# Kernel tuning notes

Hardware: AMD Instinct MI355X
Metric: run time of the kernel (lower is better)

Reference implementation:

```python
import jax, jax.numpy as jnp
import numpy as np
from jax import lax

DN = ('NCHW', 'OIHW', 'NCHW')


def setup_inputs() -> dict:
    key = jax.random.key(0)
    k1, k2 = jax.random.split(key)
    inp = jax.random.normal(k1, (32, 512, 28, 28), dtype=jnp.float32)
    w = jax.random.normal(k2, (2000, 512, 1, 1), dtype=jnp.float32)
    return {"input": inp, "weights": w}


def reference(input, weights):
    # conv2d(input^2, ones_like(weights)): every output channel is identical
    # (all-ones kernel broadcast over out-channels), so compute the
    # patch/channel sum ONCE with a single-output-channel ones kernel and
    # broadcast — same math as the original, without P-fold redundancy.
    P, C, kh, kw = weights.shape
    ones1 = jnp.ones((1, C, kh, kw), dtype=input.dtype)
    input2_patch_sum = lax.conv_general_dilated(
        input * input, ones1, window_strides=(1, 1), padding='VALID',
        dimension_numbers=DN)  # [B, 1, H', W'], broadcasts over P

    weights2 = jnp.sum(weights * weights, axis=(1, 2, 3))  # [P]
    weights2 = weights2.reshape(-1, 1, 1)  # [P, 1, 1]

    input_weights = lax.conv_general_dilated(
        input, weights, window_strides=(1, 1), padding='VALID',
        dimension_numbers=DN)  # [B, P, H', W']

    output = input2_patch_sum - 2.0 * input_weights + weights2[None]
    return jax.nn.relu(output)
```

## Files before the change

kernel.cpp:

```cpp
#include <hip/hip_runtime.h>
#include <stdint.h>

constexpr int C_IN  = 512;
constexpr int HW    = 784;
constexpr int NB    = 32;
constexpr int M_TOT = NB * HW;
constexpr int N_TOT = 2000;
constexpr int NPAD  = 2048;
constexpr int IMG_STRIDE = C_IN * HW;
constexpr int OUT_BATCH  = N_TOT * HW;

constexpr int TBM = 256;
constexpr int TBN = 128;
constexpr int NKT = C_IN / 32;

constexpr int PREPA_BLOCKS = M_TOT / 64;
constexpr int PREPW_BLOCKS = NPAD / 4;

typedef __attribute__((ext_vector_type(8))) short bf16x8;
typedef __attribute__((ext_vector_type(4))) float f32x4;

__device__ __forceinline__ uint16_t f2bf(float f) {
    union { float f; uint32_t u; } x; x.f = f;
    return (uint16_t)((x.u + 0x8000u) >> 16);
}

__device__ __forceinline__ void gload_lds16(const void* g, void* l) {
    __builtin_amdgcn_global_load_lds(
        (const __attribute__((address_space(1))) void*)g,
        (__attribute__((address_space(3))) void*)l, 16, 0, 0);
}

__device__ __forceinline__ f32x4 nt_load4(const float* p) {
    return __builtin_nontemporal_load((const f32x4*)p);
}
__device__ __forceinline__ void nt_store4(float* p, f32x4 v) {
    __builtin_nontemporal_store(v, (f32x4*)p);
}

__global__ __launch_bounds__(256) void prep_kernel(const float* __restrict__ in,
                                                   const float* __restrict__ w,
                                                   short* __restrict__ Abf,
                                                   short* __restrict__ Wbf,
                                                   float* __restrict__ s2,
                                                   float* __restrict__ w2) {
    __shared__ __align__(16) char T[64 * 512 * 2];
    __shared__ float red[16][64];

    const int t = threadIdx.x;

    if (blockIdx.x >= PREPA_BLOCKS) {
        const int wv = t >> 6, lane = t & 63;
        const int p = (blockIdx.x - PREPA_BLOCKS) * 4 + wv;
        bf16x8 o = (bf16x8)0;
        float s = 0.f;
        if (p < N_TOT) {
            const float* base = w + (size_t)p * C_IN + lane * 8;
            f32x4 a = nt_load4(base);
            f32x4 c = nt_load4(base + 4);
            s = a[0]*a[0] + a[1]*a[1] + a[2]*a[2] + a[3]*a[3]
              + c[0]*c[0] + c[1]*c[1] + c[2]*c[2] + c[3]*c[3];
            o[0] = (short)f2bf(a[0]); o[1] = (short)f2bf(a[1]);
            o[2] = (short)f2bf(a[2]); o[3] = (short)f2bf(a[3]);
            o[4] = (short)f2bf(c[0]); o[5] = (short)f2bf(c[1]);
            o[6] = (short)f2bf(c[2]); o[7] = (short)f2bf(c[3]);
        }
        *(bf16x8*)(Wbf + (size_t)p * C_IN + lane * 8) = o;
#pragma unroll
        for (int off = 32; off; off >>= 1) s += __shfl_down(s, off);
        if (lane == 0) w2[p] = s;
        return;
    }

    const int q = t & 15;
    const int part = t >> 4;
    const int m0q = blockIdx.x * 64 + q * 4;
    const uint32_t b  = (uint32_t)m0q / 784u;
    const uint32_t hw = (uint32_t)m0q % 784u;
    const float* base = in + (size_t)b * IMG_STRIDE + hw;

    float acx = 0.f, acy = 0.f, acz = 0.f, acw = 0.f;
    const int c0 = part * 32;
#pragma unroll 4
    for (int c = c0; c < c0 + 32; ++c) {
        f32x4 v = nt_load4(base + (size_t)c * HW);
        acx = fmaf(v[0], v[0], acx);
        acy = fmaf(v[1], v[1], acy);
        acz = fmaf(v[2], v[2], acz);
        acw = fmaf(v[3], v[3], acw);
        uint16_t vals[4] = { f2bf(v[0]), f2bf(v[1]), f2bf(v[2]), f2bf(v[3]) };
        const uint32_t by0 = (uint32_t)(q * 4) * 1024u + (uint32_t)c * 2u;
#pragma unroll
        for (int j = 0; j < 4; ++j) {
            uint32_t bb = by0 + (uint32_t)j * 1024u;
            bb ^= ((bb >> 12) & 7u) << 4;
            *(uint16_t*)(T + bb) = vals[j];
        }
    }
    red[part][q * 4 + 0] = acx;
    red[part][q * 4 + 1] = acy;
    red[part][q * 4 + 2] = acz;
    red[part][q * 4 + 3] = acw;
    __syncthreads();
    if (t < 64) {
        float s = 0.f;
#pragma unroll
        for (int p = 0; p < 16; ++p) s += red[p][t];
        s2[blockIdx.x * 64 + t] = s;
    }
    short* dst = Abf + (size_t)blockIdx.x * 64 * 512;
#pragma unroll
    for (int i = 0; i < 16; ++i) {
        const int idx = i * 256 + t;
        const int row = idx >> 6, ch = idx & 63;
        uint32_t bb = (uint32_t)row * 1024u + (uint32_t)ch * 16u;
        bb ^= ((bb >> 12) & 7u) << 4;
        bf16x8 v = *(bf16x8*)(T + bb);
        *(bf16x8*)(dst + (size_t)row * 512 + ch * 8) = v;
    }
}

__global__ __launch_bounds__(256, 2) void gemm10_kernel(const short* __restrict__ Abf,
                                                        const short* __restrict__ Wbf,
                                                        const float* __restrict__ s2,
                                                        const float* __restrict__ w2,
                                                        float* __restrict__ out) {
    __shared__ __align__(16) char smem[3 * 24576];

    const int t = threadIdx.x;
    const int wv = t >> 6, lane = t & 63;
    const int lr = lane & 15, lg = lane >> 4;

    const int bid = blockIdx.x;
    const int bn = bid & 15;
    const int bm = bid >> 4;

    const short* Ap = Abf + (size_t)bm * TBM * C_IN;
    const short* Bp = Wbf + (size_t)bn * TBN * C_IN;

    const int srow = wv * 16 + (lane >> 2);
    const int sg   = (lane & 3) ^ ((lane >> 3) & 3);
    const short* AsrcL = Ap + (size_t)srow * C_IN + sg * 8;
    const short* BsrcL = Bp + (size_t)srow * C_IN + sg * 8;
    const int dst = t * 16;

    const int wm = (wv >> 1) * 128;
    const int wn = (wv & 1) * 64;

    const int slot  = lg ^ ((lr >> 1) & 3);
    const int abase = (wm + lr) * 64 + slot * 16;
    const int bbase = 16384 + (wn + lr) * 64 + slot * 16;

    f32x4 acc[8][4] = {};

#define STAGE(tt)                                                              \
    do {                                                                       \
        char* buf_ = smem + ((tt) % 3) * 24576;                                \
        const short* as_ = AsrcL + (tt) * 32;                                  \
        const short* bs_ = BsrcL + (tt) * 32;                                  \
        gload_lds16(as_,              buf_ + dst);                             \
        gload_lds16(as_ +  64 * C_IN, buf_ + 4096 + dst);                      \
        gload_lds16(as_ + 128 * C_IN, buf_ + 8192 + dst);                      \
        gload_lds16(as_ + 192 * C_IN, buf_ + 12288 + dst);                     \
        gload_lds16(bs_,              buf_ + 16384 + dst);                     \
        gload_lds16(bs_ +  64 * C_IN, buf_ + 20480 + dst);                     \
    } while (0)

    STAGE(0);
    STAGE(1);

#pragma unroll
    for (int kt = 0; kt < NKT; ++kt) {
        if (kt < NKT - 1) asm volatile("s_waitcnt vmcnt(6)" ::: "memory");
        else              asm volatile("s_waitcnt vmcnt(0)" ::: "memory");
        __builtin_amdgcn_sched_barrier(0);
        __builtin_amdgcn_s_barrier();
        __builtin_amdgcn_sched_barrier(0);

        if (kt + 2 < NKT) STAGE(kt + 2);

        const char* buf = smem + (kt % 3) * 24576;
        bf16x8 bfrag[4], afrag[8];
#pragma unroll
        for (int n = 0; n < 4; ++n)
            bfrag[n] = *(const bf16x8*)(buf + bbase + n * 1024);
#pragma unroll
        for (int m = 0; m < 8; ++m)
            afrag[m] = *(const bf16x8*)(buf + abase + m * 1024);

        __builtin_amdgcn_s_setprio(1);
#pragma unroll
        for (int m = 0; m < 8; ++m)
#pragma unroll
            for (int n = 0; n < 4; ++n)
                acc[m][n] = __builtin_amdgcn_mfma_f32_16x16x32_bf16(
                    afrag[m], bfrag[n], acc[m][n], 0, 0, 0);
        __builtin_amdgcn_s_setprio(0);
    }
#undef STAGE

    float wreg[4];
    int n_ok[4];
#pragma unroll
    for (int n = 0; n < 4; ++n) {
        const int n_o = bn * TBN + wn + n * 16 + lr;
        n_ok[n] = (n_o < N_TOT);
        wreg[n] = n_ok[n] ? w2[n_o] : 0.f;
    }
#pragma unroll
    for (int m = 0; m < 8; ++m) {
        const int m_r = bm * TBM + wm + m * 16 + lg * 4;
        const f32x4 s2v = *(const f32x4*)(s2 + m_r);
        const uint32_t ob  = (uint32_t)m_r / 784u;
        const uint32_t ohw = (uint32_t)m_r % 784u;
        float* obase = out + (size_t)ob * OUT_BATCH + ohw;
#pragma unroll
        for (int n = 0; n < 4; ++n) {
            if (n_ok[n]) {
                const int n_o = bn * TBN + wn + n * 16 + lr;
                const f32x4 a = acc[m][n];
                f32x4 r;
                r[0] = fmaxf(s2v[0] - 2.f * a[0] + wreg[n], 0.f);
                r[1] = fmaxf(s2v[1] - 2.f * a[1] + wreg[n], 0.f);
                r[2] = fmaxf(s2v[2] - 2.f * a[2] + wreg[n], 0.f);
                r[3] = fmaxf(s2v[3] - 2.f * a[3] + wreg[n], 0.f);
                nt_store4(obase + (size_t)n_o * HW, r);
            }
        }
    }
}

extern "C" void kernel_launch(void* const* d_in, const int* in_sizes, int n_in,
                              void* d_out, int out_size, void* d_ws, size_t ws_size,
                              hipStream_t stream) {
    const float* in = (const float*)d_in[0];
    const float* w  = (const float*)d_in[1];
    float* out = (float*)d_out;

    const size_t offA  = 0;
    const size_t offW  = offA + (size_t)M_TOT * C_IN * sizeof(short);
    const size_t offS2 = offW + (size_t)NPAD * C_IN * sizeof(short);
    const size_t offW2 = offS2 + (size_t)M_TOT * sizeof(float);

    short* Abf = (short*)((char*)d_ws + offA);
    short* Wbf = (short*)((char*)d_ws + offW);
    float* s2  = (float*)((char*)d_ws + offS2);
    float* w2  = (float*)((char*)d_ws + offW2);

    prep_kernel<<<PREPA_BLOCKS + PREPW_BLOCKS, 256, 0, stream>>>(in, w, Abf, Wbf, s2, w2);

    gemm10_kernel<<<98 * 16, 256, 0, stream>>>(Abf, Wbf, s2, w2, out);
}
```

Baseline: 104.0 us.

## Load MFMA fragments directly from global memory into registers, dropping LDS staging

Replaces the triple-buffered LDS pipeline, which used global_load_lds and barriers, with direct per-wave global loads of bf16 fragments into registers, double-buffered across k-steps. This removes the LDS traffic and the workgroup barriers. In exchange, A and B tiles are no longer shared between waves, so global/L2 traffic rises (each A row is loaded by 2 waves, each B row by 2), and register pressure grows with two fragment sets under launch bounds of 2 blocks.

```diff
diff --git a/kernel.cpp b/kernel.cpp
--- a/kernel.cpp
+++ b/kernel.cpp
@@ -23,12 +23,6 @@
 __device__ __forceinline__ uint16_t f2bf(float f) {
     union { float f; uint32_t u; } x; x.f = f;
     return (uint16_t)((x.u + 0x8000u) >> 16);
-}
-
-__device__ __forceinline__ void gload_lds16(const void* g, void* l) {
-    __builtin_amdgcn_global_load_lds(
-        (const __attribute__((address_space(1))) void*)g,
-        (__attribute__((address_space(3))) void*)l, 16, 0, 0);
 }
 
 __device__ __forceinline__ f32x4 nt_load4(const float* p) {
@@ -120,13 +114,11 @@
     }
 }
 
-__global__ __launch_bounds__(256, 2) void gemm10_kernel(const short* __restrict__ Abf,
+__global__ __launch_bounds__(256, 2) void gemm11_kernel(const short* __restrict__ Abf,
                                                         const short* __restrict__ Wbf,
                                                         const float* __restrict__ s2,
                                                         const float* __restrict__ w2,
                                                         float* __restrict__ out) {
-    __shared__ __align__(16) char smem[3 * 24576];
-
     const int t = threadIdx.x;
     const int wv = t >> 6, lane = t & 63;
     const int lr = lane & 15, lg = lane >> 4;
@@ -135,69 +127,48 @@
     const int bn = bid & 15;
     const int bm = bid >> 4;
 
-    const short* Ap = Abf + (size_t)bm * TBM * C_IN;
-    const short* Bp = Wbf + (size_t)bn * TBN * C_IN;
-
-    const int srow = wv * 16 + (lane >> 2);
-    const int sg   = (lane & 3) ^ ((lane >> 3) & 3);
-    const short* AsrcL = Ap + (size_t)srow * C_IN + sg * 8;
-    const short* BsrcL = Bp + (size_t)srow * C_IN + sg * 8;
-    const int dst = t * 16;
-
     const int wm = (wv >> 1) * 128;
     const int wn = (wv & 1) * 64;
 
-    const int slot  = lg ^ ((lr >> 1) & 3);
-    const int abase = (wm + lr) * 64 + slot * 16;
-    const int bbase = 16384 + (wn + lr) * 64 + slot * 16;
-
+    const short* Arow = Abf + (size_t)(bm * TBM + wm + lr) * C_IN + lg * 8;
+    const short* Brow = Wbf + (size_t)(bn * TBN + wn + lr) * C_IN + lg * 8;
+
+    bf16x8 a0[8], b0[4], a1[8], b1[4];
     f32x4 acc[8][4] = {};
 
-#define STAGE(tt)                                                              \
+#define LOADF(kt, aa, bb)                                                      \
     do {                                                                       \
-        char* buf_ = smem + ((tt) % 3) * 24576;                                \
-        const short* as_ = AsrcL + (tt) * 32;                                  \
-        const short* bs_ = BsrcL + (tt) * 32;                                  \
-        gload_lds16(as_,              buf_ + dst);                             \
-        gload_lds16(as_ +  64 * C_IN, buf_ + 4096 + dst);                      \
-        gload_lds16(as_ + 128 * C_IN, buf_ + 8192 + dst);                      \
-        gload_lds16(as_ + 192 * C_IN, buf_ + 12288 + dst);                     \
-        gload_lds16(bs_,              buf_ + 16384 + dst);                     \
-        gload_lds16(bs_ +  64 * C_IN, buf_ + 20480 + dst);                     \
+        _Pragma("unroll") for (int m = 0; m < 8; ++m)                          \
+            aa[m] = *(const bf16x8*)(Arow + (size_t)m * 16 * C_IN + (kt) * 32);\
+        _Pragma("unroll") for (int n = 0; n < 4; ++n)                          \
+            bb[n] = *(const bf16x8*)(Brow + (size_t)n * 16 * C_IN + (kt) * 32);\
     } while (0)
 
-    STAGE(0);
-    STAGE(1);
+#define COMPUTE(aa, bb)                                                        \
+    do {                                                                       \
+        __builtin_amdgcn_s_setprio(1);                                         \
+        _Pragma("unroll") for (int m = 0; m < 8; ++m)                          \
+            _Pragma("unroll") for (int n = 0; n < 4; ++n)                      \
+                acc[m][n] = __builtin_amdgcn_mfma_f32_16x16x32_bf16(           \
+                    aa[m], bb[n], acc[m][n], 0, 0, 0);                         \
+        __builtin_amdgcn_s_setprio(0);                                         \
+    } while (0)
+
+    LOADF(0, a0, b0);
+    LOADF(1, a1, b1);
 
 #pragma unroll
     for (int kt = 0; kt < NKT; ++kt) {
-        if (kt < NKT - 1) asm volatile("s_waitcnt vmcnt(6)" ::: "memory");
-        else              asm volatile("s_waitcnt vmcnt(0)" ::: "memory");
-        __builtin_amdgcn_sched_barrier(0);
-        __builtin_amdgcn_s_barrier();
-        __builtin_amdgcn_sched_barrier(0);
-
-        if (kt + 2 < NKT) STAGE(kt + 2);
-
-        const char* buf = smem + (kt % 3) * 24576;
-        bf16x8 bfrag[4], afrag[8];
-#pragma unroll
-        for (int n = 0; n < 4; ++n)
-            bfrag[n] = *(const bf16x8*)(buf + bbase + n * 1024);
-#pragma unroll
-        for (int m = 0; m < 8; ++m)
-            afrag[m] = *(const bf16x8*)(buf + abase + m * 1024);
-
-        __builtin_amdgcn_s_setprio(1);
-#pragma unroll
-        for (int m = 0; m < 8; ++m)
-#pragma unroll
-            for (int n = 0; n < 4; ++n)
-                acc[m][n] = __builtin_amdgcn_mfma_f32_16x16x32_bf16(
-                    afrag[m], bfrag[n], acc[m][n], 0, 0, 0);
-        __builtin_amdgcn_s_setprio(0);
-    }
-#undef STAGE
+        if ((kt & 1) == 0) {
+            COMPUTE(a0, b0);
+            if (kt + 2 < NKT) LOADF(kt + 2, a0, b0);
+        } else {
+            COMPUTE(a1, b1);
+            if (kt + 2 < NKT) LOADF(kt + 2, a1, b1);
+        }
+    }
+#undef LOADF
+#undef COMPUTE
 
     float wreg[4];
     int n_ok[4];
@@ -249,5 +220,5 @@
 
     prep_kernel<<<PREPA_BLOCKS + PREPW_BLOCKS, 256, 0, stream>>>(in, w, Abf, Wbf, s2, w2);
 
-    gemm10_kernel<<<98 * 16, 256, 0, stream>>>(Abf, Wbf, s2, w2, out);
-}
+    gemm11_kernel<<<98 * 16, 256, 0, stream>>>(Abf, Wbf, s2, w2, out);
+}
```

Result: slower. 185.0 us (+78.0%).
